# Performance work log

Hardware: AMD Instinct MI355X
Metric: run time of the kernel (lower is better)

The kernel has to match this reference:

```python
import math
import jax, jax.numpy as jnp
import numpy as np

DIM = 256
HEADS = 8
WS = (8, 8)   # window_size
SS = (4, 4)   # shift_size


def _rel_tables():
    """Static SwinV2 continuous relative-position coordinate table and index."""
    wh, ww = WS
    ch = np.arange(-(wh - 1), wh, dtype=np.float32)
    cw = np.arange(-(ww - 1), ww, dtype=np.float32)
    table = np.stack(np.meshgrid(ch, cw, indexing='ij'), axis=-1)  # (2wh-1, 2ww-1, 2)
    table[..., 0] /= (wh - 1)
    table[..., 1] /= (ww - 1)
    table *= 8.0
    table = np.sign(table) * np.log2(np.abs(table) + 1.0) / 3.0
    coords = np.stack(np.meshgrid(np.arange(wh), np.arange(ww), indexing='ij'))
    cf = coords.reshape(2, -1)                      # (2, N)
    rel = (cf[:, :, None] - cf[:, None, :]).transpose(1, 2, 0)  # (N, N, 2)
    rel[..., 0] += wh - 1
    rel[..., 1] += ww - 1
    rel[..., 0] *= 2 * ww - 1
    idx = rel.sum(-1).reshape(-1)                   # (N*N,)
    return jnp.asarray(table, jnp.float32), jnp.asarray(idx, jnp.int32)


def _attn_mask(pad_H, pad_W, sh, sw):
    """Static shifted-window attention mask, shape (num_windows, N, N)."""
    wh, ww = WS
    m = np.zeros((pad_H, pad_W), np.float32)
    cnt = 0
    for hs in ((0, -wh), (-wh, -sh), (-sh, None)):
        for ws_ in ((0, -ww), (-ww, -sw), (-sw, None)):
            m[hs[0]:hs[1], ws_[0]:ws_[1]] = cnt
            cnt += 1
    m = m.reshape(pad_H // wh, wh, pad_W // ww, ww).transpose(0, 2, 1, 3)
    m = m.reshape(-1, wh * ww)                      # (nW, N)
    diff = m[:, None, :] - m[:, :, None]            # (nW, N, N)
    return jnp.asarray(np.where(diff != 0, -100.0, 0.0).astype(np.float32))


def setup_inputs() -> dict:
    key = jax.random.key(0)
    ks = jax.random.split(key, 12)
    C, Hh = DIM, HEADS
    s = 0.02
    inp = {
        'x': jax.random.normal(ks[0], (16, 64, 64, C), jnp.float32),
        'Wq': jax.random.normal(ks[1], (C, C), jnp.float32) * s,
        'bq': jnp.zeros((C,), jnp.float32),
        'Wk': jax.random.normal(ks[2], (C, C), jnp.float32) * s,
        'bk': jnp.zeros((C,), jnp.float32),
        'Wv': jax.random.normal(ks[3], (C, C), jnp.float32) * s,
        'bv': jnp.zeros((C,), jnp.float32),
        'Wo': jax.random.normal(ks[4], (C, C), jnp.float32) * s,
        'bo': jnp.zeros((C,), jnp.float32),
        'logit_scale': jnp.full((Hh, 1, 1), math.log(10.0), jnp.float32),
        'cpb_w1': jax.random.normal(ks[5], (2, 512), jnp.float32) * s,
        'cpb_b1': jnp.zeros((512,), jnp.float32),
        'cpb_w2': jax.random.normal(ks[6], (512, Hh), jnp.float32) * s,
    }
    return inp


def reference(x, Wq, bq, Wk, bk, Wv, bv, Wo, bo, logit_scale, cpb_w1, cpb_b1, cpb_w2):
    B, H, W, C = x.shape
    wh, ww = WS
    hd = C // HEADS
    pad_b = (wh - H % wh) % wh
    pad_r = (ww - W % ww) % ww
    x = jnp.pad(x, ((0, 0), (0, pad_b), (0, pad_r), (0, 0)))
    pH, pW = H + pad_b, W + pad_r
    sh = 0 if wh >= pH else SS[0]
    sw = 0 if ww >= pW else SS[1]

    xs = jnp.roll(x, (-sh, -sw), axis=(1, 2))
    nW = (pH // wh) * (pW // ww)
    N = wh * ww
    # window partition -> (B*nW, N, C)
    xw = xs.reshape(B, pH // wh, wh, pW // ww, ww, C).transpose(0, 1, 3, 2, 4, 5)
    xw = xw.reshape(B * nW, N, C)

    def heads(t):
        return t.reshape(B * nW, N, HEADS, hd).transpose(0, 2, 1, 3)  # (BnW, H, N, hd)

    q = heads(xw @ Wq + bq)
    k = heads(xw @ Wk + bk)
    v = heads(xw @ Wv + bv)

    # cosine attention (F.normalize, eps=1e-12)
    qn = q / jnp.maximum(jnp.linalg.norm(q, axis=-1, keepdims=True), 1e-12)
    kn = k / jnp.maximum(jnp.linalg.norm(k, axis=-1, keepdims=True), 1e-12)
    attn = jnp.einsum('bhnd,bhmd->bhnm', qn, kn)

    scale = jnp.exp(jnp.minimum(logit_scale, math.log(100.0)))  # (HEADS,1,1)
    attn = attn * scale[None]

    table, idx = _rel_tables()
    bias = jax.nn.relu(table @ cpb_w1 + cpb_b1) @ cpb_w2        # (2wh-1, 2ww-1, HEADS)
    bias = bias.reshape(-1, HEADS)[idx].reshape(N, N, HEADS).transpose(2, 0, 1)
    attn = attn + (16.0 * jax.nn.sigmoid(bias))[None]

    if sh + sw > 0:
        mask = _attn_mask(pH, pW, sh, sw)                        # (nW, N, N)
        attn = attn.reshape(B, nW, HEADS, N, N) + mask[None, :, None]
        attn = attn.reshape(B * nW, HEADS, N, N)

    attn = jax.nn.softmax(attn, axis=-1)
    out = jnp.einsum('bhnm,bhmd->bhnd', attn, v)
    out = out.transpose(0, 2, 1, 3).reshape(B * nW, N, C)
    out = out @ Wo + bo

    out = out.reshape(B, pH // wh, pW // ww, wh, ww, C).transpose(0, 1, 3, 2, 4, 5)
    out = out.reshape(B, pH, pW, C)
    if sh + sw > 0:
        out = jnp.roll(out, (sh, sw), axis=(1, 2))
    return out[:, :H, :W, :]
```

## Files before the change

kernel.cpp:

```cpp
#include <hip/hip_runtime.h>
#include <hip/hip_bf16.h>

typedef float floatx4 __attribute__((ext_vector_type(4)));
typedef short shortx8 __attribute__((ext_vector_type(8)));
typedef short shortx4 __attribute__((ext_vector_type(4)));

#define CFENCE() asm volatile("" ::: "memory")

__device__ __forceinline__ float bf2f(short s) {
    union { unsigned u; float f; } cv;
    cv.u = ((unsigned)(unsigned short)s) << 16;
    return cv.f;
}
__device__ __forceinline__ short f2bf(float f) {
    union { float f; unsigned u; } cv; cv.f = f;
    unsigned r = (cv.u + 0x7fffu + ((cv.u >> 16) & 1u)) >> 16;
    return (short)r;
}

__global__ __launch_bounds__(256) void wtrans(const float* __restrict__ Wq,
                                              const float* __restrict__ Wk,
                                              const float* __restrict__ Wv,
                                              const float* __restrict__ Wo,
                                              short* __restrict__ wqkv_t,
                                              short* __restrict__ wo_t) {
    __shared__ float tile[32][33];
    int z = blockIdx.z;
    const float* src = (z == 0) ? Wq : (z == 1) ? Wk : (z == 2) ? Wv : Wo;
    int n0 = blockIdx.x * 32, k0 = blockIdx.y * 32;
    for (int p = threadIdx.y; p < 32; p += 8)
        tile[p][threadIdx.x] = src[(size_t)(k0 + p) * 256 + n0 + threadIdx.x];
    __syncthreads();
    for (int p = threadIdx.y; p < 32; p += 8) {
        int n = n0 + p, k = k0 + threadIdx.x;
        short b = f2bf(tile[threadIdx.x][p]);
        if (z < 3) wqkv_t[(size_t)(z * 256 + n) * 256 + k] = b;
        else       wo_t[(size_t)n * 256 + k] = b;
    }
}

__device__ __forceinline__ float sgnlog(float x) {
    return copysignf(__log2f(fabsf(x) + 1.f) / 3.f, x);
}
__global__ __launch_bounds__(256) void bias_mlp(const float* __restrict__ ls,
                                                const float* __restrict__ w1,
                                                const float* __restrict__ b1,
                                                const float* __restrict__ w2,
                                                float* __restrict__ b225g,
                                                float* __restrict__ scaleOut) {
    int e = blockIdx.x;
    int tid = threadIdx.x, lane = tid & 63, wid = tid >> 6;
    if (e == 0 && tid < 8) scaleOut[tid] = expf(fminf(ls[tid], 4.6051701859880914f));
    int dh = e / 15 - 7, dw = e % 15 - 7;
    float t0 = sgnlog(8.f * (float)dh / 7.f);
    float t1 = sgnlog(8.f * (float)dw / 7.f);
    float acc[8];
#pragma unroll
    for (int j = 0; j < 8; ++j) acc[j] = 0.f;
#pragma unroll
    for (int s = 0; s < 2; ++s) {
        int hsm = tid + s * 256;
        float hid = fmaxf(0.f, t0 * w1[hsm] + t1 * w1[512 + hsm] + b1[hsm]);
#pragma unroll
        for (int j = 0; j < 8; ++j) acc[j] += hid * w2[hsm * 8 + j];
    }
#pragma unroll
    for (int off = 1; off < 64; off <<= 1)
#pragma unroll
        for (int j = 0; j < 8; ++j) acc[j] += __shfl_xor(acc[j], off, 64);
    __shared__ float red[4][8];
    if (lane == 0)
#pragma unroll
        for (int j = 0; j < 8; ++j) red[wid][j] = acc[j];
    __syncthreads();
    if (tid < 8)
        b225g[e * 8 + tid] = red[0][tid] + red[1][tid] + red[2][tid] + red[3][tid];
}

__global__ __launch_bounds__(256) void bias_expand(const float* __restrict__ b225g,
                                                   float* __restrict__ bias8) {
    int f = blockIdx.x * 256 + threadIdx.x;
    int h = f >> 12, ij = f & 4095, i = ij >> 6, j = ij & 63;
    int dh = (i >> 3) - (j >> 3), dw = (i & 7) - (j & 7);
    int e = (dh + 7) * 15 + (dw + 7);
    float v = b225g[e * 8 + h];
    bias8[f] = 16.f / (1.f + expf(-v));
}

__device__ __forceinline__ int row2pix(int row) {
    int w = row >> 6, t = row & 63;
    int b = w >> 6, wi = (w >> 3) & 7, wj = w & 7;
    int hh = (wi * 8 + (t >> 3) + 4) & 63;
    int ww = (wj * 8 + (t & 7) + 4) & 63;
    return (b * 64 + hh) * 64 + ww;
}

__global__ __launch_bounds__(256, 2) void qkv_gemm(const float* __restrict__ x,
                                                   const short* __restrict__ wt,
                                                   const float* __restrict__ bq,
                                                   const float* __restrict__ bk_,
                                                   const float* __restrict__ bv,
                                                   short* __restrict__ qkv) {
    __shared__ __align__(16) short As[128 * 264];
    __shared__ __align__(16) short Bs[128 * 40];
    int tid = threadIdx.x, lane = tid & 63, wid = tid >> 6;
    int quad = lane >> 4, l15 = lane & 15;
    int bm = blockIdx.x;

    {
        int r = tid >> 1, half = tid & 1;
        const float* src = x + (size_t)row2pix(bm * 128 + r) * 256 + half * 128;
        short* dst = &As[r * 264 + half * 128];
#pragma unroll
        for (int g = 0; g < 4; ++g) {
            float4 v[8];
#pragma unroll
            for (int j = 0; j < 8; ++j) v[j] = *(const float4*)(src + g * 32 + j * 4);
#pragma unroll
            for (int j = 0; j < 4; ++j) {
                shortx8 s;
#pragma unroll
                for (int q2 = 0; q2 < 2; ++q2) {
                    float4 f = v[j * 2 + q2];
                    s[q2 * 4 + 0] = f2bf(f.x); s[q2 * 4 + 1] = f2bf(f.y);
                    s[q2 * 4 + 2] = f2bf(f.z); s[q2 * 4 + 3] = f2bf(f.w);
                }
                *(shortx8*)(dst + g * 32 + j * 8) = s;
            }
        }
    }

    int br = tid >> 1, bc = tid & 1;
    shortx8 pf0, pf1;
    {
        const short* p = wt + (size_t)br * 256 + bc * 16;
        pf0 = *(const shortx8*)p; pf1 = *(const shortx8*)(p + 8);
    }
    int wm = (wid & 1) * 64, wn = (wid >> 1) * 64;

    for (int t = 0; t < 6; ++t) {
        floatx4 acc[4][4];
#pragma unroll
        for (int mt = 0; mt < 4; ++mt)
#pragma unroll
            for (int nt = 0; nt < 4; ++nt) acc[mt][nt] = (floatx4){0.f, 0.f, 0.f, 0.f};
        for (int kt = 0; kt < 8; ++kt) {
            __syncthreads();
            *(shortx8*)&Bs[br * 40 + bc * 16] = pf0;
            *(shortx8*)&Bs[br * 40 + bc * 16 + 8] = pf1;
            __syncthreads();
            int nt_ = t, nkt = kt + 1;
            if (nkt == 8) { nt_ = t + 1; nkt = 0; }
            if (nt_ < 6) {
                const short* p = wt + (size_t)(nt_ * 128 + br) * 256 + nkt * 32 + bc * 16;
                pf0 = *(const shortx8*)p; pf1 = *(const shortx8*)(p + 8);
            }
            shortx8 af[4], bfr[4];
#pragma unroll
            for (int mt = 0; mt < 4; ++mt)
                af[mt] = *(const shortx8*)&As[(wm + mt * 16 + l15) * 264 + kt * 32 + quad * 8];
#pragma unroll
            for (int nt = 0; nt < 4; ++nt)
                bfr[nt] = *(const shortx8*)&Bs[(wn + nt * 16 + l15) * 40 + quad * 8];
#pragma unroll
            for (int mt = 0; mt < 4; ++mt)
#pragma unroll
                for (int nt = 0; nt < 4; ++nt)
                    acc[mt][nt] = __builtin_amdgcn_mfma_f32_16x16x32_bf16(af[mt], bfr[nt], acc[mt][nt], 0, 0, 0);
        }
        float biasv[4];
#pragma unroll
        for (int nt = 0; nt < 4; ++nt) {
            int col = t * 128 + wn + nt * 16 + l15;
            biasv[nt] = (col < 256) ? bq[col] : (col < 512) ? bk_[col - 256] : bv[col - 512];
        }
#pragma unroll
        for (int mt = 0; mt < 4; ++mt)
#pragma unroll
            for (int nt = 0; nt < 4; ++nt)
#pragma unroll
                for (int reg = 0; reg < 4; ++reg) {
                    int row = bm * 128 + wm + mt * 16 + quad * 4 + reg;
                    int col = t * 128 + wn + nt * 16 + l15;
                    qkv[(size_t)row * 768 + col] = f2bf(acc[mt][nt][reg] + biasv[nt]);
                }
    }
}

__device__ __forceinline__ int regid(int t, int wi, int wj) {
    int a = (wi < 7) ? 0 : (((t >> 3) < 4) ? 1 : 2);
    int b = (wj < 7) ? 0 : (((t & 7) < 4) ? 1 : 2);
    return a * 3 + b;
}

__global__ __launch_bounds__(256, 2) void attn_kernel(const short* __restrict__ qkv,
                                                      const float* __restrict__ bias8,
                                                      const float* __restrict__ scale,
                                                      short* __restrict__ aout) {
    __shared__ __align__(16) short lds[4 * 8192];
    int tid = threadIdx.x, lane = tid & 63, wid = tid >> 6;
    int quad = lane >> 4, l15 = lane & 15;
    int win = blockIdx.x;
    int wi = (win >> 3) & 7, wj = win & 7;
    bool need_mask = (wi == 7) || (wj == 7);
    short* qn = &lds[wid * 8192];
    short* kn = qn + 3584;
    short* P = qn;
    short* vt = qn + 5632;

    for (int hi = 0; hi < 2; ++hi) {
        int h = wid + hi * 4;
        float sc = scale[h];
        const short* qp = qkv + (size_t)(win * 64 + lane) * 768 + h * 32;
        shortx8 qraw[4], kraw[4], vraw[4];
#pragma unroll
        for (int c2 = 0; c2 < 4; ++c2) {
            qraw[c2] = *(const shortx8*)(qp + c2 * 8);
            kraw[c2] = *(const shortx8*)(qp + 256 + c2 * 8);
            vraw[c2] = *(const shortx8*)(qp + 512 + c2 * 8);
        }
        float qs = 0.f, ks2 = 0.f;
#pragma unroll
        for (int c2 = 0; c2 < 4; ++c2)
#pragma unroll
            for (int j = 0; j < 8; ++j) {
                float f = bf2f(qraw[c2][j]); qs += f * f;
                float g = bf2f(kraw[c2][j]); ks2 += g * g;
            }
        float qr = sc / fmaxf(sqrtf(qs), 1e-12f);
        float kr = 1.f / fmaxf(sqrtf(ks2), 1e-12f);
        CFENCE();
#pragma unroll
        for (int c2 = 0; c2 < 4; ++c2) {
            shortx8 oq, ok;
#pragma unroll
            for (int j = 0; j < 8; ++j) {
                oq[j] = f2bf(bf2f(qraw[c2][j]) * qr);
                ok[j] = f2bf(bf2f(kraw[c2][j]) * kr);
            }
            *(shortx8*)&qn[lane * 56 + c2 * 8] = oq;
            *(shortx8*)&kn[lane * 56 + c2 * 8] = ok;
        }
        CFENCE();
        shortx8 aq[4], bkf[4];
#pragma unroll
        for (int mt = 0; mt < 4; ++mt)
            aq[mt] = *(const shortx8*)&qn[(mt * 16 + l15) * 56 + quad * 8];
#pragma unroll
        for (int nt = 0; nt < 4; ++nt)
            bkf[nt] = *(const shortx8*)&kn[(nt * 16 + l15) * 56 + quad * 8];
        floatx4 S[4][4];
#pragma unroll
        for (int mt = 0; mt < 4; ++mt)
#pragma unroll
            for (int nt = 0; nt < 4; ++nt) {
                floatx4 z = {0.f, 0.f, 0.f, 0.f};
                S[mt][nt] = __builtin_amdgcn_mfma_f32_16x16x32_bf16(aq[mt], bkf[nt], z, 0, 0, 0);
            }
        const float* bh = bias8 + (h << 12);
        float bound = sc + 16.5f;
        int jid[4];
        if (need_mask) {
#pragma unroll
            for (int nt = 0; nt < 4; ++nt) jid[nt] = regid(nt * 16 + l15, wi, wj);
        }
        float rs[4][4];
#pragma unroll
        for (int mt = 0; mt < 4; ++mt)
#pragma unroll
            for (int reg = 0; reg < 4; ++reg) {
                int i = mt * 16 + quad * 4 + reg;
                int iid = need_mask ? regid(i, wi, wj) : 0;
                float rowsum = 0.f;
#pragma unroll
                for (int nt = 0; nt < 4; ++nt) {
                    int j = nt * 16 + l15;
                    float v = S[mt][nt][reg] + bh[i * 64 + j];
                    if (need_mask && iid != jid[nt]) v -= 100.f;
                    float p = __expf(v - bound);
                    S[mt][nt][reg] = p;
                    rowsum += p;
                }
                rowsum += __shfl_xor(rowsum, 1, 64);
                rowsum += __shfl_xor(rowsum, 2, 64);
                rowsum += __shfl_xor(rowsum, 4, 64);
                rowsum += __shfl_xor(rowsum, 8, 64);
                rs[mt][reg] = 1.f / rowsum;
            }
        CFENCE();
#pragma unroll
        for (int mt = 0; mt < 4; ++mt)
#pragma unroll
            for (int nt = 0; nt < 4; ++nt)
#pragma unroll
                for (int reg = 0; reg < 4; ++reg)
                    P[(mt * 16 + quad * 4 + reg) * 88 + nt * 16 + l15] = f2bf(S[mt][nt][reg]);
#pragma unroll
        for (int c2 = 0; c2 < 4; ++c2)
#pragma unroll
            for (int j = 0; j < 8; ++j)
                vt[(c2 * 8 + j) * 72 + lane] = vraw[c2][j];
        CFENCE();
        floatx4 O[4][2];
#pragma unroll
        for (int mt = 0; mt < 4; ++mt)
#pragma unroll
            for (int nt = 0; nt < 2; ++nt) O[mt][nt] = (floatx4){0.f, 0.f, 0.f, 0.f};
#pragma unroll
        for (int ks = 0; ks < 2; ++ks) {
            shortx8 pa[4], vb[2];
#pragma unroll
            for (int mt = 0; mt < 4; ++mt)
                pa[mt] = *(const shortx8*)&P[(mt * 16 + l15) * 88 + ks * 32 + quad * 8];
#pragma unroll
            for (int nt = 0; nt < 2; ++nt)
                vb[nt] = *(const shortx8*)&vt[(nt * 16 + l15) * 72 + ks * 32 + quad * 8];
#pragma unroll
            for (int mt = 0; mt < 4; ++mt)
#pragma unroll
                for (int nt = 0; nt < 2; ++nt)
                    O[mt][nt] = __builtin_amdgcn_mfma_f32_16x16x32_bf16(pa[mt], vb[nt], O[mt][nt], 0, 0, 0);
        }
#pragma unroll
        for (int mt = 0; mt < 4; ++mt)
#pragma unroll
            for (int nt = 0; nt < 2; ++nt)
#pragma unroll
                for (int reg = 0; reg < 4; ++reg) {
                    int i = mt * 16 + quad * 4 + reg;
                    int d = nt * 16 + l15;
                    aout[(size_t)(win * 64 + i) * 256 + (h << 5) + d] =
                        f2bf(O[mt][nt][reg] * rs[mt][reg]);
                }
    }
}

__global__ __launch_bounds__(256, 2) void oproj_gemm(const short* __restrict__ ao,
                                                     const short* __restrict__ wot,
                                                     const float* __restrict__ bo,
                                                     float* __restrict__ out) {
    __shared__ __align__(16) short As[128 * 264];
    __shared__ __align__(16) short Bs[128 * 40];
    int tid = threadIdx.x, lane = tid & 63, wid = tid >> 6;
    int quad = lane >> 4, l15 = lane & 15;
    int bm = blockIdx.x;

    {
        int r = tid >> 1, half = tid & 1;
        const short* src = ao + (size_t)(bm * 128 + r) * 256 + half * 128;
        short* dst = &As[r * 264 + half * 128];
#pragma unroll
        for (int g = 0; g < 2; ++g) {
            shortx8 v[8];
#pragma unroll
            for (int j = 0; j < 8; ++j) v[j] = *(const shortx8*)(src + g * 64 + j * 8);
#pragma unroll
            for (int j = 0; j < 8; ++j) *(shortx8*)(dst + g * 64 + j * 8) = v[j];
        }
    }

    int br = tid >> 1, bc = tid & 1;
    shortx8 pf0, pf1;
    {
        const short* p = wot + (size_t)br * 256 + bc * 16;
        pf0 = *(const shortx8*)p; pf1 = *(const shortx8*)(p + 8);
    }
    int wm = (wid & 1) * 64, wn = (wid >> 1) * 64;

    for (int t = 0; t < 2; ++t) {
        floatx4 acc[4][4];
#pragma unroll
        for (int mt = 0; mt < 4; ++mt)
#pragma unroll
            for (int nt = 0; nt < 4; ++nt) acc[mt][nt] = (floatx4){0.f, 0.f, 0.f, 0.f};
        for (int kt = 0; kt < 8; ++kt) {
            __syncthreads();
            *(shortx8*)&Bs[br * 40 + bc * 16] = pf0;
            *(shortx8*)&Bs[br * 40 + bc * 16 + 8] = pf1;
            __syncthreads();
            int nt_ = t, nkt = kt + 1;
            if (nkt == 8) { nt_ = t + 1; nkt = 0; }
            if (nt_ < 2) {
                const short* p = wot + (size_t)(nt_ * 128 + br) * 256 + nkt * 32 + bc * 16;
                pf0 = *(const shortx8*)p; pf1 = *(const shortx8*)(p + 8);
            }
            shortx8 af[4], bfr[4];
#pragma unroll
            for (int mt = 0; mt < 4; ++mt)
                af[mt] = *(const shortx8*)&As[(wm + mt * 16 + l15) * 264 + kt * 32 + quad * 8];
#pragma unroll
            for (int nt = 0; nt < 4; ++nt)
                bfr[nt] = *(const shortx8*)&Bs[(wn + nt * 16 + l15) * 40 + quad * 8];
#pragma unroll
            for (int mt = 0; mt < 4; ++mt)
#pragma unroll
                for (int nt = 0; nt < 4; ++nt)
                    acc[mt][nt] = __builtin_amdgcn_mfma_f32_16x16x32_bf16(af[mt], bfr[nt], acc[mt][nt], 0, 0, 0);
        }
        float biasv[4];
#pragma unroll
        for (int nt = 0; nt < 4; ++nt) biasv[nt] = bo[t * 128 + wn + nt * 16 + l15];
#pragma unroll
        for (int mt = 0; mt < 4; ++mt)
#pragma unroll
            for (int nt = 0; nt < 4; ++nt)
#pragma unroll
                for (int reg = 0; reg < 4; ++reg) {
                    int row = bm * 128 + wm + mt * 16 + quad * 4 + reg;
                    int col = t * 128 + wn + nt * 16 + l15;
                    out[(size_t)row2pix(row) * 256 + col] = acc[mt][nt][reg] + biasv[nt];
                }
    }
}

extern "C" void kernel_launch(void* const* d_in, const int* in_sizes, int n_in,
                              void* d_out, int out_size, void* d_ws, size_t ws_size,
                              hipStream_t stream) {
    const float* x  = (const float*)d_in[0];
    const float* Wq = (const float*)d_in[1];
    const float* bq = (const float*)d_in[2];
    const float* Wk = (const float*)d_in[3];
    const float* bk = (const float*)d_in[4];
    const float* Wv = (const float*)d_in[5];
    const float* bv = (const float*)d_in[6];
    const float* Wo = (const float*)d_in[7];
    const float* bo = (const float*)d_in[8];
    const float* ls = (const float*)d_in[9];
    const float* w1 = (const float*)d_in[10];
    const float* b1 = (const float*)d_in[11];
    const float* w2 = (const float*)d_in[12];

    char* ws = (char*)d_ws;
    short* wqkv_t = (short*)(ws + 0);
    short* wo_t   = (short*)(ws + 393216);
    float* bias8  = (float*)(ws + 524288);
    float* scale  = (float*)(ws + 655360);
    float* b225g  = (float*)(ws + 786432);
    short* qkv    = (short*)(ws + 1048576);
    short* aout   = (short*)(ws + 101711872);
    float* out    = (float*)d_out;

    hipLaunchKernelGGL(wtrans, dim3(8, 8, 4), dim3(32, 8), 0, stream, Wq, Wk, Wv, Wo, wqkv_t, wo_t);
    hipLaunchKernelGGL(bias_mlp, dim3(225), dim3(256), 0, stream, ls, w1, b1, w2, b225g, scale);
    hipLaunchKernelGGL(bias_expand, dim3(128), dim3(256), 0, stream, b225g, bias8);
    hipLaunchKernelGGL(qkv_gemm, dim3(512), dim3(256), 0, stream, x, wqkv_t, bq, bk, bv, qkv);
    hipLaunchKernelGGL(attn_kernel, dim3(1024), dim3(256), 0, stream, qkv, bias8, scale, aout);
    hipLaunchKernelGGL(oproj_gemm, dim3(512), dim3(256), 0, stream, aout, wo_t, bo, out);
}
```

Baseline: 248.3 us.

## Load GEMM weight fragments directly from global into registers, dropping LDS staging

```diff
diff --git a/kernel.cpp b/kernel.cpp
--- a/kernel.cpp
+++ b/kernel.cpp
@@ -102,7 +102,6 @@
                                                    const float* __restrict__ bv,
                                                    short* __restrict__ qkv) {
     __shared__ __align__(16) short As[128 * 264];
-    __shared__ __align__(16) short Bs[128 * 40];
     int tid = threadIdx.x, lane = tid & 63, wid = tid >> 6;
     int quad = lane >> 4, l15 = lane & 15;
     int bm = blockIdx.x;
@@ -130,13 +129,19 @@
         }
     }
 
-    int br = tid >> 1, bc = tid & 1;
-    shortx8 pf0, pf1;
-    {
-        const short* p = wt + (size_t)br * 256 + bc * 16;
-        pf0 = *(const shortx8*)p; pf1 = *(const shortx8*)(p + 8);
-    }
     int wm = (wid & 1) * 64, wn = (wid >> 1) * 64;
+    const short* bbase[4];
+#pragma unroll
+    for (int nt = 0; nt < 4; ++nt)
+        bbase[nt] = wt + (size_t)(wn + nt * 16 + l15) * 256 + quad * 8;
+
+    shortx8 b0[4], b1[4];
+#pragma unroll
+    for (int nt = 0; nt < 4; ++nt) b0[nt] = *(const shortx8*)(bbase[nt] + 0);
+#pragma unroll
+    for (int nt = 0; nt < 4; ++nt) b1[nt] = *(const shortx8*)(bbase[nt] + 32);
+
+    __syncthreads();
 
     for (int t = 0; t < 6; ++t) {
         floatx4 acc[4][4];
@@ -144,29 +149,27 @@
         for (int mt = 0; mt < 4; ++mt)
 #pragma unroll
             for (int nt = 0; nt < 4; ++nt) acc[mt][nt] = (floatx4){0.f, 0.f, 0.f, 0.f};
+#pragma unroll
         for (int kt = 0; kt < 8; ++kt) {
-            __syncthreads();
-            *(shortx8*)&Bs[br * 40 + bc * 16] = pf0;
-            *(shortx8*)&Bs[br * 40 + bc * 16 + 8] = pf1;
-            __syncthreads();
-            int nt_ = t, nkt = kt + 1;
-            if (nkt == 8) { nt_ = t + 1; nkt = 0; }
-            if (nt_ < 6) {
-                const short* p = wt + (size_t)(nt_ * 128 + br) * 256 + nkt * 32 + bc * 16;
-                pf0 = *(const shortx8*)p; pf1 = *(const shortx8*)(p + 8);
-            }
-            shortx8 af[4], bfr[4];
+            int u = t * 8 + kt + 2;
+            shortx8 bn[4];
+            if (u < 48) {
+                int tn = u >> 3, kn = u & 7;
+#pragma unroll
+                for (int nt = 0; nt < 4; ++nt)
+                    bn[nt] = *(const shortx8*)(bbase[nt] + tn * 32768 + kn * 32);
+            }
+            shortx8 af[4];
 #pragma unroll
             for (int mt = 0; mt < 4; ++mt)
                 af[mt] = *(const shortx8*)&As[(wm + mt * 16 + l15) * 264 + kt * 32 + quad * 8];
 #pragma unroll
-            for (int nt = 0; nt < 4; ++nt)
-                bfr[nt] = *(const shortx8*)&Bs[(wn + nt * 16 + l15) * 40 + quad * 8];
-#pragma unroll
             for (int mt = 0; mt < 4; ++mt)
 #pragma unroll
                 for (int nt = 0; nt < 4; ++nt)
-                    acc[mt][nt] = __builtin_amdgcn_mfma_f32_16x16x32_bf16(af[mt], bfr[nt], acc[mt][nt], 0, 0, 0);
+                    acc[mt][nt] = __builtin_amdgcn_mfma_f32_16x16x32_bf16(af[mt], b0[nt], acc[mt][nt], 0, 0, 0);
+#pragma unroll
+            for (int nt = 0; nt < 4; ++nt) { b0[nt] = b1[nt]; b1[nt] = bn[nt]; }
         }
         float biasv[4];
 #pragma unroll
@@ -340,7 +343,6 @@
                                                      const float* __restrict__ bo,
                                                      float* __restrict__ out) {
     __shared__ __align__(16) short As[128 * 264];
-    __shared__ __align__(16) short Bs[128 * 40];
     int tid = threadIdx.x, lane = tid & 63, wid = tid >> 6;
     int quad = lane >> 4, l15 = lane & 15;
     int bm = blockIdx.x;
@@ -359,13 +361,19 @@
         }
     }
 
-    int br = tid >> 1, bc = tid & 1;
-    shortx8 pf0, pf1;
-    {
-        const short* p = wot + (size_t)br * 256 + bc * 16;
-        pf0 = *(const shortx8*)p; pf1 = *(const shortx8*)(p + 8);
-    }
     int wm = (wid & 1) * 64, wn = (wid >> 1) * 64;
+    const short* bbase[4];
+#pragma unroll
+    for (int nt = 0; nt < 4; ++nt)
+        bbase[nt] = wot + (size_t)(wn + nt * 16 + l15) * 256 + quad * 8;
+
+    shortx8 b0[4], b1[4];
+#pragma unroll
+    for (int nt = 0; nt < 4; ++nt) b0[nt] = *(const shortx8*)(bbase[nt] + 0);
+#pragma unroll
+    for (int nt = 0; nt < 4; ++nt) b1[nt] = *(const shortx8*)(bbase[nt] + 32);
+
+    __syncthreads();
 
     for (int t = 0; t < 2; ++t) {
         floatx4 acc[4][4];
@@ -373,29 +381,27 @@
         for (int mt = 0; mt < 4; ++mt)
 #pragma unroll
             for (int nt = 0; nt < 4; ++nt) acc[mt][nt] = (floatx4){0.f, 0.f, 0.f, 0.f};
+#pragma unroll
         for (int kt = 0; kt < 8; ++kt) {
-            __syncthreads();
-            *(shortx8*)&Bs[br * 40 + bc * 16] = pf0;
-            *(shortx8*)&Bs[br * 40 + bc * 16 + 8] = pf1;
-            __syncthreads();
-            int nt_ = t, nkt = kt + 1;
-            if (nkt == 8) { nt_ = t + 1; nkt = 0; }
-            if (nt_ < 2) {
-                const short* p = wot + (size_t)(nt_ * 128 + br) * 256 + nkt * 32 + bc * 16;
-                pf0 = *(const shortx8*)p; pf1 = *(const shortx8*)(p + 8);
-            }
-            shortx8 af[4], bfr[4];
+            int u = t * 8 + kt + 2;
+            shortx8 bn[4];
+            if (u < 16) {
+                int tn = u >> 3, kn = u & 7;
+#pragma unroll
+                for (int nt = 0; nt < 4; ++nt)
+                    bn[nt] = *(const shortx8*)(bbase[nt] + tn * 32768 + kn * 32);
+            }
+            shortx8 af[4];
 #pragma unroll
             for (int mt = 0; mt < 4; ++mt)
                 af[mt] = *(const shortx8*)&As[(wm + mt * 16 + l15) * 264 + kt * 32 + quad * 8];
 #pragma unroll
-            for (int nt = 0; nt < 4; ++nt)
-                bfr[nt] = *(const shortx8*)&Bs[(wn + nt * 16 + l15) * 40 + quad * 8];
-#pragma unroll
             for (int mt = 0; mt < 4; ++mt)
 #pragma unroll
                 for (int nt = 0; nt < 4; ++nt)
-                    acc[mt][nt] = __builtin_amdgcn_mfma_f32_16x16x32_bf16(af[mt], bfr[nt], acc[mt][nt], 0, 0, 0);
+                    acc[mt][nt] = __builtin_amdgcn_mfma_f32_16x16x32_bf16(af[mt], b0[nt], acc[mt][nt], 0, 0, 0);
+#pragma unroll
+            for (int nt = 0; nt < 4; ++nt) { b0[nt] = b1[nt]; b1[nt] = bn[nt]; }
         }
         float biasv[4];
 #pragma unroll
```

After: 307.9 us. 24.0% more time.
